# Optimization experiments

Hardware: AMD Instinct MI355X
Metric: run time of the kernel (lower is better)

The kernel has to match this reference:

```python
import jax, jax.numpy as jnp
import numpy as np

B, T, A, I, H = 256, 128, 4, 128, 256


def setup_inputs() -> dict:
    key = jax.random.key(0)
    ks = jax.random.split(key, 6)
    x = jax.random.normal(ks[0], (B, T, A, I), jnp.float32)
    is_init = jax.random.randint(ks[1], (B, T, 1), 0, 2).astype(bool)
    s = 1.0 / np.sqrt(H)  # torch GRUCell init range
    W_ih = jax.random.uniform(ks[2], (3 * H, I), jnp.float32, -s, s)
    W_hh = jax.random.uniform(ks[3], (3 * H, H), jnp.float32, -s, s)
    b_ih = jax.random.uniform(ks[4], (3 * H,), jnp.float32, -s, s)
    b_hh = jax.random.uniform(ks[5], (3 * H,), jnp.float32, -s, s)
    return dict(x=x, is_init=is_init, W_ih=W_ih, W_hh=W_hh, b_ih=b_ih, b_hh=b_hh)


def _gru_forward(x, is_init, W_ih, W_hh, b_ih, b_hh):
    Bb, Tt, Aa, Ii = x.shape
    Hh = W_hh.shape[1]
    # Precompute input projections for all steps: [B,T,A,3H]
    gi = jnp.einsum('btai,ki->btak', x, W_ih) + b_ih
    # is_init [B,T,1] -> per-agent reset mask [B,T,A,1]
    init = jnp.broadcast_to(is_init[:, :, None, :], (Bb, Tt, Aa, 1))
    h0 = jnp.zeros((Bb, Aa, Hh), x.dtype)

    def step(h, inp):
        gi_t, init_t = inp  # [B,A,3H], [B,A,1]
        h = jnp.where(init_t, 0.0, h)  # per-step reset before the cell
        gh = jnp.einsum('bah,kh->bak', h, W_hh) + b_hh
        i_r, i_z, i_n = jnp.split(gi_t, 3, axis=-1)
        h_r, h_z, h_n = jnp.split(gh, 3, axis=-1)
        r = jax.nn.sigmoid(i_r + h_r)
        z = jax.nn.sigmoid(i_z + h_z)
        n = jnp.tanh(i_n + r * h_n)
        h_new = (1.0 - z) * n + z * h
        return h_new, h_new

    _, hs = jax.lax.scan(step, h0, (jnp.moveaxis(gi, 1, 0), jnp.moveaxis(init, 1, 0)))
    return jnp.moveaxis(hs, 0, 1)  # [B,T,A,H]


def reference(x, is_init, W_ih, W_hh, b_ih, b_hh):
    output = _gru_forward(x, is_init, W_ih, W_hh, b_ih, b_hh)
    h_n = output[:, -1]  # [B,A,H]
    return (output, h_n)
```

## Files before the change

### kernel.cpp

```cpp
#include <hip/hip_runtime.h>
#include <cstdint>
#include <cstddef>

#define BB 256
#define TT 128
#define AA 4
#define II 128
#define HH 256
#define K3 768

typedef __attribute__((ext_vector_type(8))) short short8;
typedef __attribute__((ext_vector_type(4))) float f32x4;
typedef __attribute__((ext_vector_type(4))) unsigned short ushort4_t;

#define LGKM_BARRIER() asm volatile("s_waitcnt lgkmcnt(0)\n\ts_barrier" ::: "memory")

static __device__ __forceinline__ unsigned short f2bf(float f) {
  unsigned int b = __float_as_uint(f);
  return (unsigned short)((b + 0x7FFFu + ((b >> 16) & 1u)) >> 16);
}
static __device__ __forceinline__ float bf2f(unsigned short u) {
  return __uint_as_float(((unsigned int)u) << 16);
}

__global__ void wconv_kernel(const float* __restrict__ wih,
                             const float* __restrict__ whh,
                             unsigned short* __restrict__ o) {
  int i = blockIdx.x * 512 + threadIdx.x;
  float v = (i < K3 * II) ? wih[i] : whh[i - K3 * II];
  o[i] = f2bf(v);
}

__global__ __launch_bounds__(512, 2) void gi_kernel(
    const float* __restrict__ x,
    const float* __restrict__ bih_g,
    const float* __restrict__ bhh_g,
    const unsigned short* __restrict__ wb,
    unsigned short* __restrict__ gi) {
  __shared__ alignas(16) unsigned short xs[64][144];
  __shared__ alignas(16) unsigned short gst[16][792];
  __shared__ float bihs[K3];

  const int tid = threadIdx.x;
  const int l = tid & 63, w = tid >> 6;
  const int c = l & 15, g = l >> 4;
  const size_t m0 = (size_t)blockIdx.x * 64;

  for (int i = tid; i < K3; i += 512)
    bihs[i] = bih_g[i] + (i < 2 * HH ? bhh_g[i] : 0.f);
  for (int i = tid; i < 64 * 128; i += 512) {
    int row = i >> 7, col = i & 127;
    xs[row][col] = f2bf(x[m0 * 128 + i]);
  }
  short8 wf[6][4];
#pragma unroll
  for (int kt = 0; kt < 6; ++kt) {
    int row = 96 * w + kt * 16 + c;
#pragma unroll
    for (int kk = 0; kk < 4; ++kk)
      wf[kt][kk] = *(const short8*)&wb[(size_t)row * II + kk * 32 + g * 8];
  }
  LGKM_BARRIER();

  for (int chunk = 0; chunk < 4; ++chunk) {
    short8 bx[4];
#pragma unroll
    for (int kk = 0; kk < 4; ++kk)
      bx[kk] = *(const short8*)&xs[chunk * 16 + c][kk * 32 + g * 8];
    f32x4 acc[6];
#pragma unroll
    for (int kt = 0; kt < 6; ++kt) acc[kt] = (f32x4){0.f, 0.f, 0.f, 0.f};
#pragma unroll
    for (int kt = 0; kt < 6; ++kt)
#pragma unroll
      for (int kk = 0; kk < 4; ++kk)
        acc[kt] = __builtin_amdgcn_mfma_f32_16x16x32_bf16(wf[kt][kk], bx[kk], acc[kt], 0, 0, 0);
#pragma unroll
    for (int kt = 0; kt < 6; ++kt) {
      int gate0 = 96 * w + kt * 16 + g * 4;
      ushort4_t p;
#pragma unroll
      for (int r = 0; r < 4; ++r) p[r] = f2bf(acc[kt][r] + bihs[gate0 + r]);
      *(ushort4_t*)&gst[c][gate0] = p;
    }
    LGKM_BARRIER();
    for (int i = tid; i < 16 * 96; i += 512) {
      int row = i / 96, seg = i - row * 96;
      *(short8*)(gi + (m0 + chunk * 16 + row) * K3 + seg * 8) =
          *(const short8*)&gst[row][seg * 8];
    }
    LGKM_BARRIER();
  }
}

__global__ __launch_bounds__(512, 2) void rnn_kernel(
    const void* __restrict__ init_raw,
    const float* __restrict__ bhh_g,
    const unsigned short* __restrict__ wsb,
    const unsigned short* __restrict__ gi,
    float* __restrict__ out) {
  extern __shared__ char smem[];
  unsigned short* wlN = (unsigned short*)smem;
  unsigned short* hsb = (unsigned short*)(smem + 131072);
  unsigned char* mskL = (unsigned char*)(smem + 147456);
  int* bnd = (int*)(smem + 147592);
  int* detf = (int*)(smem + 147612);

  const int tid = threadIdx.x;
  const int b = blockIdx.x;
  const unsigned short* whh_b = wsb + K3 * II;

  if (tid < 3) detf[tid] = 0;
  for (int i = tid; i < 8192; i += 512) hsb[i] = 0;
  for (int f = tid; f < 8192; f += 512) {
    int w2 = f >> 10, n = (f >> 9) & 1, kk = (f >> 6) & 7, l2 = f & 63;
    int row = 512 + 32 * w2 + 16 * n + (l2 & 15);
    int col = kk * 32 + (l2 >> 4) * 8;
    *(short8*)(wlN + (size_t)f * 8) = *(const short8*)&whh_b[(size_t)row * HH + col];
  }

  {
    const unsigned int* wq = (const unsigned int*)init_raw;
    int notf = 0, gt1 = 0, oddnz = 0;
    for (int i = tid; i < (BB * TT / 4); i += 512) {
      unsigned int v = wq[i];
      notf |= (v != 0u && v != 0x3F800000u);
      gt1 |= (v > 1u);
      if (i & 1) oddnz |= (v != 0u);
    }
    if (notf) atomicOr(&detf[0], 1);
    if (gt1) atomicOr(&detf[1], 1);
    if (oddnz) atomicOr(&detf[2], 1);
  }
  __syncthreads();
  if (tid < TT) {
    int layout = (!detf[0]) ? 1 : (detf[1] ? 0 : (detf[2] ? 1 : 2));
    int e = b * TT + tid;
    unsigned int v;
    if (layout == 0)      v = ((const unsigned char*)init_raw)[e];
    else if (layout == 1) v = ((const unsigned int*)init_raw)[e];
    else                  v = ((const unsigned int*)init_raw)[2 * e];
    mskL[tid] = v ? 1 : 0;
  }
  if (tid == TT) mskL[TT] = 1;
  __syncthreads();
  if (tid < 3) {
    int target = 32 * (tid + 1);
    int bb = TT;
    for (int t = target; t < TT; ++t)
      if (mskL[t]) { bb = t; break; }
    bnd[tid + 1] = bb;
  }
  if (tid == 3) { bnd[0] = 0; bnd[4] = TT; }

  const int l = tid & 63, w = tid >> 6;
  const int c = l & 15, g = l >> 4;

  short8 wreg[4][8];
#pragma unroll
  for (int q = 0; q < 4; ++q) {
    int row = (q >> 1) * 256 + 32 * w + (q & 1) * 16 + c;
#pragma unroll
    for (int kk = 0; kk < 8; ++kk)
      wreg[q][kk] = *(const short8*)&whh_b[(size_t)row * HH + kk * 32 + g * 8];
  }
  __syncthreads();

  const int a = c & 3, q = c >> 2;
  const int j0 = 32 * w + g * 4;
  int tcur = bnd[q];
  int trem = bnd[q + 1] - tcur;
  int maxlen = bnd[1] - bnd[0];
  { int l1 = bnd[2] - bnd[1]; if (l1 > maxlen) maxlen = l1;
    int l2 = bnd[3] - bnd[2]; if (l2 > maxlen) maxlen = l2;
    int l3 = TT - bnd[3];     if (l3 > maxlen) maxlen = l3; }
  const int taddr = (tcur < TT) ? tcur : (TT - 1);
  const unsigned short* gp = gi + ((size_t)(b * TT + taddr) * AA + a) * K3 + j0;
  float* op = out + ((size_t)(b * TT + taddr) * AA + a) * HH + j0;
  f32x4 bn[2];
  bn[0] = *(const f32x4*)&bhh_g[2 * HH + j0];
  bn[1] = *(const f32x4*)&bhh_g[2 * HH + j0 + 16];
  float* hnp = out + (size_t)BB * TT * AA * HH + ((size_t)b * AA + a) * HH + j0;

  const unsigned short* hrd = hsb + c * 32 + g * 8;
  unsigned short* hw1 = hsb + w * 512 + c * 32 + (g >> 1) * 8 + (g & 1) * 4;
  const unsigned short* wlp = wlN + w * 8192 + l * 8;

  f32x4 hold[2];
  hold[0] = (f32x4){0.f, 0.f, 0.f, 0.f};
  hold[1] = (f32x4){0.f, 0.f, 0.f, 0.f};
  const f32x4 Z4 = {0.f, 0.f, 0.f, 0.f};

#define L2E 1.44269504088896f

#define STEP(P)                                                                   \
  do {                                                                            \
    ushort4_t gr0 = *(const ushort4_t*)(gp);                                      \
    ushort4_t gr1 = *(const ushort4_t*)(gp + 16);                                 \
    ushort4_t gz0 = *(const ushort4_t*)(gp + 256);                                \
    ushort4_t gz1 = *(const ushort4_t*)(gp + 272);                                \
    ushort4_t gn0 = *(const ushort4_t*)(gp + 512);                                \
    ushort4_t gn1 = *(const ushort4_t*)(gp + 528);                                \
    short8 bhf[8];                                                                \
    _Pragma("unroll") for (int kk = 0; kk < 8; ++kk)                              \
        bhf[kk] = *(const short8*)(hrd + (P) * 4096 + kk * 512);                  \
    f32x4 aR0 = __builtin_amdgcn_mfma_f32_16x16x32_bf16(wreg[0][0], bhf[0], Z4, 0, 0, 0); \
    f32x4 aR1 = __builtin_amdgcn_mfma_f32_16x16x32_bf16(wreg[1][0], bhf[0], Z4, 0, 0, 0); \
    f32x4 aZ0 = __builtin_amdgcn_mfma_f32_16x16x32_bf16(wreg[2][0], bhf[0], Z4, 0, 0, 0); \
    f32x4 aZ1 = __builtin_amdgcn_mfma_f32_16x16x32_bf16(wreg[3][0], bhf[0], Z4, 0, 0, 0); \
    f32x4 aN0 = __builtin_amdgcn_mfma_f32_16x16x32_bf16(*(const short8*)(wlp), bhf[0], Z4, 0, 0, 0); \
    f32x4 aN1 = __builtin_amdgcn_mfma_f32_16x16x32_bf16(*(const short8*)(wlp + 4096), bhf[0], Z4, 0, 0, 0); \
    _Pragma("unroll") for (int kk = 1; kk < 8; ++kk) {                            \
      aR0 = __builtin_amdgcn_mfma_f32_16x16x32_bf16(wreg[0][kk], bhf[kk], aR0, 0, 0, 0); \
      aR1 = __builtin_amdgcn_mfma_f32_16x16x32_bf16(wreg[1][kk], bhf[kk], aR1, 0, 0, 0); \
      aZ0 = __builtin_amdgcn_mfma_f32_16x16x32_bf16(wreg[2][kk], bhf[kk], aZ0, 0, 0, 0); \
      aZ1 = __builtin_amdgcn_mfma_f32_16x16x32_bf16(wreg[3][kk], bhf[kk], aZ1, 0, 0, 0); \
      aN0 = __builtin_amdgcn_mfma_f32_16x16x32_bf16(*(const short8*)(wlp + kk * 512), bhf[kk], aN0, 0, 0, 0); \
      aN1 = __builtin_amdgcn_mfma_f32_16x16x32_bf16(*(const short8*)(wlp + 4096 + kk * 512), bhf[kk], aN1, 0, 0, 0); \
    }                                                                             \
    f32x4 hnv0, hnv1;                                                             \
    ushort4_t hb0, hb1;                                                           \
    _Pragma("unroll") for (int r = 0; r < 4; ++r) {                               \
      const float pr = bf2f(gr0[r]) + aR0[r];                                     \
      const float pz = bf2f(gz0[r]) + aZ0[r];                                     \
      const float rs = __builtin_amdgcn_rcpf(1.f + __builtin_amdgcn_exp2f(-pr * L2E)); \
      const float zs = __builtin_amdgcn_rcpf(1.f + __builtin_amdgcn_exp2f(-pz * L2E)); \
      const float hn = aN0[r] + bn[0][r];                                         \
      const float pre = bf2f(gn0[r]) + rs * hn;                                   \
      const float nn = 1.f - 2.f * __builtin_amdgcn_rcpf(1.f + __builtin_amdgcn_exp2f(pre * (2.f * L2E))); \
      const float hv = fmaf(zs, hold[0][r] - nn, nn);                             \
      hnv0[r] = hv; hb0[r] = f2bf(hv);                                            \
    }                                                                             \
    _Pragma("unroll") for (int r = 0; r < 4; ++r) {                               \
      const float pr = bf2f(gr1[r]) + aR1[r];                                     \
      const float pz = bf2f(gz1[r]) + aZ1[r];                                     \
      const float rs = __builtin_amdgcn_rcpf(1.f + __builtin_amdgcn_exp2f(-pr * L2E)); \
      const float zs = __builtin_amdgcn_rcpf(1.f + __builtin_amdgcn_exp2f(-pz * L2E)); \
      const float hn = aN1[r] + bn[1][r];                                         \
      const float pre = bf2f(gn1[r]) + rs * hn;                                   \
      const float nn = 1.f - 2.f * __builtin_amdgcn_rcpf(1.f + __builtin_amdgcn_exp2f(pre * (2.f * L2E))); \
      const float hv = fmaf(zs, hold[1][r] - nn, nn);                             \
      hnv1[r] = hv; hb1[r] = f2bf(hv);                                            \
    }                                                                             \
    hold[0] = hnv0; hold[1] = hnv1;                                               \
    const bool active = (trem > 0);                                               \
    if (active) {                                                                 \
      *(f32x4*)op = hnv0;                                                         \
      *(f32x4*)(op + 16) = hnv1;                                                  \
      if (tcur == TT - 1) { *(f32x4*)hnp = hnv0; *(f32x4*)(hnp + 16) = hnv1; }    \
      tcur += 1; trem -= 1;                                                       \
      if (trem > 0) { gp += AA * K3; op += AA * HH; }                             \
    }                                                                             \
    const int mn = mskL[tcur];                                                    \
    if (mn) {                                                                     \
      hb0 = (ushort4_t)0; hb1 = (ushort4_t)0;                                     \
      hold[0] = Z4; hold[1] = Z4;                                                 \
    }                                                                             \
    *(ushort4_t*)(hw1 + (1 - (P)) * 4096) = hb0;                                  \
    *(ushort4_t*)(hw1 + 16 + (1 - (P)) * 4096) = hb1;                             \
    LGKM_BARRIER();                                                               \
  } while (0)

  const int nsteps = (maxlen + 1) & ~1;
  for (int i = 0; i < nsteps; i += 2) {
    STEP(0);
    STEP(1);
  }
#undef STEP
}

template <int WSW>
__global__ __launch_bounds__(512, 2) void gru_kernel(
    const float* __restrict__ x,
    const void* __restrict__ init_raw,
    const float* __restrict__ wih_f,
    const float* __restrict__ whh_f,
    const float* __restrict__ bih_g,
    const float* __restrict__ bhh_g,
    const unsigned short* __restrict__ wb,
    float* __restrict__ out) {
  __shared__ alignas(16) unsigned short xs[AA][II + 8];
  __shared__ alignas(16) unsigned short hsb[AA][HH + 8];
  __shared__ float hs32[AA][HH];
  __shared__ float gi_s[K3][5];
  __shared__ float gh_s[K3][5];
  __shared__ float bihs[K3];
  __shared__ float bhhs[K3];
  __shared__ unsigned char msk[TT];
  __shared__ int detf[3];

  const int tid = threadIdx.x;
  const int b = blockIdx.x;

  if (tid < 3) detf[tid] = 0;
  for (int i = tid; i < K3; i += 512) { bihs[i] = bih_g[i]; bhhs[i] = bhh_g[i]; }
  for (int i = tid; i < AA * HH; i += 512) {
    hs32[i >> 8][i & 255] = 0.f;
    hsb[i >> 8][i & 255] = 0;
  }
  __syncthreads();
  {
    const unsigned int* wq = (const unsigned int*)init_raw;
    int notf = 0, gt1 = 0, oddnz = 0;
    for (int i = tid; i < (BB * TT / 4); i += 512) {
      unsigned int v = wq[i];
      notf |= (v != 0u && v != 0x3F800000u);
      gt1 |= (v > 1u);
      if (i & 1) oddnz |= (v != 0u);
    }
    if (notf) atomicOr(&detf[0], 1);
    if (gt1) atomicOr(&detf[1], 1);
    if (oddnz) atomicOr(&detf[2], 1);
  }
  __syncthreads();
  if (tid < TT) {
    int layout = (!detf[0]) ? 1 : (detf[1] ? 0 : (detf[2] ? 1 : 2));
    int e = b * TT + tid;
    unsigned int v;
    if (layout == 0)      v = ((const unsigned char*)init_raw)[e];
    else if (layout == 1) v = ((const unsigned int*)init_raw)[e];
    else                  v = ((const unsigned int*)init_raw)[2 * e];
    msk[tid] = v ? 1 : 0;
  }
  __syncthreads();

  const int l = tid & 63;
  const int w = tid >> 6;
  const int c = l & 15;
  const int g = l >> 4;
  const bool act = (c < AA);
  const int xa = tid >> 7, xi = tid & 127;
  const float* xrow = x + (size_t)b * TT * AA * II;
  const unsigned short* wihb = wb;
  const unsigned short* whhb = wb + K3 * II;

  for (int t = 0; t < TT; ++t) {
    xs[xa][xi] = f2bf(xrow[(size_t)t * (AA * II) + tid]);
    if (msk[t]) {
      for (int i = tid; i < AA * HH; i += 512) {
        hs32[i >> 8][i & 255] = 0.f;
        hsb[i >> 8][i & 255] = 0;
      }
    }
    __syncthreads();

    short8 bx[4], bh[8];
    if (act) {
#pragma unroll
      for (int kk = 0; kk < 4; ++kk) bx[kk] = *(const short8*)&xs[c][kk * 32 + g * 8];
#pragma unroll
      for (int kk = 0; kk < 8; ++kk) bh[kk] = *(const short8*)&hsb[c][kk * 32 + g * 8];
    } else {
#pragma unroll
      for (int kk = 0; kk < 4; ++kk) bx[kk] = (short8)0;
#pragma unroll
      for (int kk = 0; kk < 8; ++kk) bh[kk] = (short8)0;
    }

#pragma unroll
    for (int kt = 0; kt < 6; ++kt) {
      const int ar = w * 96 + kt * 16 + c;
      f32x4 acc = {0.f, 0.f, 0.f, 0.f};
#pragma unroll
      for (int kk = 0; kk < 4; ++kk) {
        short8 aw;
        if (WSW) {
          aw = *(const short8*)&wihb[(size_t)ar * II + kk * 32 + g * 8];
        } else {
          const float* p = &wih_f[(size_t)ar * II + kk * 32 + g * 8];
#pragma unroll
          for (int e = 0; e < 8; ++e) aw[e] = (short)f2bf(p[e]);
        }
        acc = __builtin_amdgcn_mfma_f32_16x16x32_bf16(aw, bx[kk], acc, 0, 0, 0);
      }
      if (act) {
        const int dr = w * 96 + kt * 16 + g * 4;
#pragma unroll
        for (int r = 0; r < 4; ++r) gi_s[dr + r][c] = acc[r];
      }
    }

#pragma unroll
    for (int kt = 0; kt < 6; ++kt) {
      const int ar = w * 96 + kt * 16 + c;
      f32x4 acc = {0.f, 0.f, 0.f, 0.f};
#pragma unroll
      for (int kk = 0; kk < 8; ++kk) {
        short8 aw;
        if (WSW) {
          aw = *(const short8*)&whhb[(size_t)ar * HH + kk * 32 + g * 8];
        } else {
          const float* p = &whh_f[(size_t)ar * HH + kk * 32 + g * 8];
#pragma unroll
          for (int e = 0; e < 8; ++e) aw[e] = (short)f2bf(p[e]);
        }
        acc = __builtin_amdgcn_mfma_f32_16x16x32_bf16(aw, bh[kk], acc, 0, 0, 0);
      }
      if (act) {
        const int dr = w * 96 + kt * 16 + g * 4;
#pragma unroll
        for (int r = 0; r < 4; ++r) gh_s[dr + r][c] = acc[r];
      }
    }
    __syncthreads();

#pragma unroll
    for (int it = 0; it < 2; ++it) {
      const int idx = it * 512 + tid;
      const int a = idx >> 8, j = idx & 255;
      const float ir = gi_s[j][a] + bihs[j];
      const float iz = gi_s[HH + j][a] + bihs[HH + j];
      const float inn = gi_s[2 * HH + j][a] + bihs[2 * HH + j];
      const float hr = gh_s[j][a] + bhhs[j];
      const float hz = gh_s[HH + j][a] + bhhs[HH + j];
      const float hn = gh_s[2 * HH + j][a] + bhhs[2 * HH + j];
      const float r = 1.f / (1.f + __expf(-(ir + hr)));
      const float z = 1.f / (1.f + __expf(-(iz + hz)));
      const float pre = inn + r * hn;
      const float ea = __expf(-2.f * fabsf(pre));
      float n = (1.f - ea) / (1.f + ea);
      n = (pre < 0.f) ? -n : n;
      const float hold = hs32[a][j];
      const float hnew = (1.f - z) * n + z * hold;
      hs32[a][j] = hnew;
      hsb[a][j] = f2bf(hnew);
      out[(((size_t)b * TT + t) * AA + a) * HH + j] = hnew;
      if (t == TT - 1)
        out[(size_t)BB * TT * AA * HH + ((size_t)b * AA + a) * HH + j] = hnew;
    }
    __syncthreads();
  }
}

extern "C" void kernel_launch(void* const* d_in, const int* in_sizes, int n_in,
                              void* d_out, int out_size, void* d_ws, size_t ws_size,
                              hipStream_t stream) {
  (void)in_sizes; (void)n_in; (void)out_size;
  const float* x = (const float*)d_in[0];
  const void* is_init = d_in[1];
  const float* wih = (const float*)d_in[2];
  const float* whh = (const float*)d_in[3];
  const float* bih = (const float*)d_in[4];
  const float* bhh = (const float*)d_in[5];
  float* out = (float*)d_out;

  const size_t W_ELS = (size_t)(K3 * II + K3 * HH);
  const size_t W_BYTES = W_ELS * 2;
  const size_t GI_BYTES = (size_t)BB * TT * AA * K3 * 2;
  const int SMEM = 147632;

  if (ws_size >= W_BYTES + GI_BYTES) {
    hipError_t e = hipFuncSetAttribute(
        (const void*)rnn_kernel, hipFuncAttributeMaxDynamicSharedMemorySize, SMEM);
    if (e == hipSuccess) {
      unsigned short* wb = (unsigned short*)d_ws;
      unsigned short* gi = wb + W_ELS;
      wconv_kernel<<<(int)(W_ELS / 512), 512, 0, stream>>>(wih, whh, wb);
      gi_kernel<<<2048, 512, 0, stream>>>(x, bih, bhh, wb, gi);
      rnn_kernel<<<BB, 512, SMEM, stream>>>(is_init, bhh, wb, gi, out);
      return;
    }
  }
  if (ws_size >= W_BYTES) {
    unsigned short* wb = (unsigned short*)d_ws;
    wconv_kernel<<<(int)(W_ELS / 512), 512, 0, stream>>>(wih, whh, wb);
    gru_kernel<1><<<BB, 512, 0, stream>>>(x, is_init, wih, whh, bih, bhh, wb, out);
  } else {
    gru_kernel<0><<<BB, 512, 0, stream>>>(x, is_init, wih, whh, bih, bhh, nullptr, out);
  }
}
```

Before: 246.6 us.

## Stream pre-swizzled n-gate W_hh fragments from global instead of staging in LDS

```diff
diff --git a/kernel.cpp b/kernel.cpp
--- a/kernel.cpp
+++ b/kernel.cpp
@@ -29,6 +29,15 @@
   int i = blockIdx.x * 512 + threadIdx.x;
   float v = (i < K3 * II) ? wih[i] : whh[i - K3 * II];
   o[i] = f2bf(v);
+}
+
+__global__ void wfrag_kernel(const unsigned short* __restrict__ whh_b,
+                             unsigned short* __restrict__ dst) {
+  int f = blockIdx.x * 512 + threadIdx.x;
+  int w2 = f >> 10, n = (f >> 9) & 1, kk = (f >> 6) & 7, l2 = f & 63;
+  int row = 512 + 32 * w2 + 16 * n + (l2 & 15);
+  int col = kk * 32 + (l2 >> 4) * 8;
+  *(short8*)(dst + (size_t)f * 8) = *(const short8*)&whh_b[(size_t)row * HH + col];
 }
 
 __global__ __launch_bounds__(512, 2) void gi_kernel(
@@ -98,26 +107,19 @@
     const float* __restrict__ bhh_g,
     const unsigned short* __restrict__ wsb,
     const unsigned short* __restrict__ gi,
+    const unsigned short* __restrict__ wfN,
     float* __restrict__ out) {
-  extern __shared__ char smem[];
-  unsigned short* wlN = (unsigned short*)smem;
-  unsigned short* hsb = (unsigned short*)(smem + 131072);
-  unsigned char* mskL = (unsigned char*)(smem + 147456);
-  int* bnd = (int*)(smem + 147592);
-  int* detf = (int*)(smem + 147612);
+  __shared__ alignas(16) unsigned short hsb[2][4096];
+  __shared__ unsigned char mskL[132];
+  __shared__ int bnd[5];
+  __shared__ int detf[3];
 
   const int tid = threadIdx.x;
   const int b = blockIdx.x;
   const unsigned short* whh_b = wsb + K3 * II;
 
   if (tid < 3) detf[tid] = 0;
-  for (int i = tid; i < 8192; i += 512) hsb[i] = 0;
-  for (int f = tid; f < 8192; f += 512) {
-    int w2 = f >> 10, n = (f >> 9) & 1, kk = (f >> 6) & 7, l2 = f & 63;
-    int row = 512 + 32 * w2 + 16 * n + (l2 & 15);
-    int col = kk * 32 + (l2 >> 4) * 8;
-    *(short8*)(wlN + (size_t)f * 8) = *(const short8*)&whh_b[(size_t)row * HH + col];
-  }
+  for (int i = tid; i < 8192; i += 512) (&hsb[0][0])[i] = 0;
 
   {
     const unsigned int* wq = (const unsigned int*)init_raw;
@@ -182,9 +184,10 @@
   bn[1] = *(const f32x4*)&bhh_g[2 * HH + j0 + 16];
   float* hnp = out + (size_t)BB * TT * AA * HH + ((size_t)b * AA + a) * HH + j0;
 
-  const unsigned short* hrd = hsb + c * 32 + g * 8;
-  unsigned short* hw1 = hsb + w * 512 + c * 32 + (g >> 1) * 8 + (g & 1) * 4;
-  const unsigned short* wlp = wlN + w * 8192 + l * 8;
+  unsigned short* hflat = &hsb[0][0];
+  const unsigned short* hrd = hflat + l * 8;
+  unsigned short* hw1 = hflat + w * 512 + (g >> 1) * 128 + c * 8 + (g & 1) * 4;
+  const unsigned short* wgp = wfN + w * 8192 + l * 8;
 
   f32x4 hold[2];
   hold[0] = (f32x4){0.f, 0.f, 0.f, 0.f};
@@ -208,15 +211,15 @@
     f32x4 aR1 = __builtin_amdgcn_mfma_f32_16x16x32_bf16(wreg[1][0], bhf[0], Z4, 0, 0, 0); \
     f32x4 aZ0 = __builtin_amdgcn_mfma_f32_16x16x32_bf16(wreg[2][0], bhf[0], Z4, 0, 0, 0); \
     f32x4 aZ1 = __builtin_amdgcn_mfma_f32_16x16x32_bf16(wreg[3][0], bhf[0], Z4, 0, 0, 0); \
-    f32x4 aN0 = __builtin_amdgcn_mfma_f32_16x16x32_bf16(*(const short8*)(wlp), bhf[0], Z4, 0, 0, 0); \
-    f32x4 aN1 = __builtin_amdgcn_mfma_f32_16x16x32_bf16(*(const short8*)(wlp + 4096), bhf[0], Z4, 0, 0, 0); \
+    f32x4 aN0 = __builtin_amdgcn_mfma_f32_16x16x32_bf16(*(const short8*)(wgp), bhf[0], Z4, 0, 0, 0); \
+    f32x4 aN1 = __builtin_amdgcn_mfma_f32_16x16x32_bf16(*(const short8*)(wgp + 4096), bhf[0], Z4, 0, 0, 0); \
     _Pragma("unroll") for (int kk = 1; kk < 8; ++kk) {                            \
       aR0 = __builtin_amdgcn_mfma_f32_16x16x32_bf16(wreg[0][kk], bhf[kk], aR0, 0, 0, 0); \
       aR1 = __builtin_amdgcn_mfma_f32_16x16x32_bf16(wreg[1][kk], bhf[kk], aR1, 0, 0, 0); \
       aZ0 = __builtin_amdgcn_mfma_f32_16x16x32_bf16(wreg[2][kk], bhf[kk], aZ0, 0, 0, 0); \
       aZ1 = __builtin_amdgcn_mfma_f32_16x16x32_bf16(wreg[3][kk], bhf[kk], aZ1, 0, 0, 0); \
-      aN0 = __builtin_amdgcn_mfma_f32_16x16x32_bf16(*(const short8*)(wlp + kk * 512), bhf[kk], aN0, 0, 0, 0); \
-      aN1 = __builtin_amdgcn_mfma_f32_16x16x32_bf16(*(const short8*)(wlp + 4096 + kk * 512), bhf[kk], aN1, 0, 0, 0); \
+      aN0 = __builtin_amdgcn_mfma_f32_16x16x32_bf16(*(const short8*)(wgp + kk * 512), bhf[kk], aN0, 0, 0, 0); \
+      aN1 = __builtin_amdgcn_mfma_f32_16x16x32_bf16(*(const short8*)(wgp + 4096 + kk * 512), bhf[kk], aN1, 0, 0, 0); \
     }                                                                             \
     f32x4 hnv0, hnv1;                                                             \
     ushort4_t hb0, hb1;                                                           \
@@ -257,7 +260,7 @@
       hold[0] = Z4; hold[1] = Z4;                                                 \
     }                                                                             \
     *(ushort4_t*)(hw1 + (1 - (P)) * 4096) = hb0;                                  \
-    *(ushort4_t*)(hw1 + 16 + (1 - (P)) * 4096) = hb1;                             \
+    *(ushort4_t*)(hw1 + 256 + (1 - (P)) * 4096) = hb1;                            \
     LGKM_BARRIER();                                                               \
   } while (0)
 
@@ -447,19 +450,15 @@
   const size_t W_ELS = (size_t)(K3 * II + K3 * HH);
   const size_t W_BYTES = W_ELS * 2;
   const size_t GI_BYTES = (size_t)BB * TT * AA * K3 * 2;
-  const int SMEM = 147632;
 
   if (ws_size >= W_BYTES + GI_BYTES) {
-    hipError_t e = hipFuncSetAttribute(
-        (const void*)rnn_kernel, hipFuncAttributeMaxDynamicSharedMemorySize, SMEM);
-    if (e == hipSuccess) {
-      unsigned short* wb = (unsigned short*)d_ws;
-      unsigned short* gi = wb + W_ELS;
-      wconv_kernel<<<(int)(W_ELS / 512), 512, 0, stream>>>(wih, whh, wb);
-      gi_kernel<<<2048, 512, 0, stream>>>(x, bih, bhh, wb, gi);
-      rnn_kernel<<<BB, 512, SMEM, stream>>>(is_init, bhh, wb, gi, out);
-      return;
-    }
+    unsigned short* wb = (unsigned short*)d_ws;
+    unsigned short* gi = wb + W_ELS;
+    wconv_kernel<<<(int)(W_ELS / 512), 512, 0, stream>>>(wih, whh, wb);
+    gi_kernel<<<2048, 512, 0, stream>>>(x, bih, bhh, wb, gi);
+    wfrag_kernel<<<16, 512, 0, stream>>>(wb + K3 * II, wb);
+    rnn_kernel<<<BB, 512, 0, stream>>>(is_init, bhh, wb, gi, wb, out);
+    return;
   }
   if (ws_size >= W_BYTES) {
     unsigned short* wb = (unsigned short*)d_ws;
```

Result: slower. 373.4 us (+51.4%).
